# Optimization experiments

Hardware: AMD Instinct MI355X
Metric: run time of the kernel (lower is better)

The kernel has to match this reference:

```python
import jax, jax.numpy as jnp
import numpy as np
from jax import lax

B, N = 16, 4096
NPOINT, RADIUS, NSAMPLE = 1024, 0.2, 32
BN_EPS = 1e-5
MLP_DIMS = [(64, 6), (64, 64), (128, 64)]  # (C_out, C_in)


def setup_inputs() -> dict:
    key = jax.random.key(0)
    ks = jax.random.split(key, 2 + len(MLP_DIMS))
    inp = {
        "xyz": jax.random.uniform(ks[0], (B, 3, N), jnp.float32),   # unit cube
        "points": jax.random.normal(ks[1], (B, 3, N), jnp.float32),  # extra features, D=3
    }
    for i, (co, ci) in enumerate(MLP_DIMS):
        inp[f"conv_w{i}"] = jax.random.normal(ks[2 + i], (co, ci), jnp.float32) * 0.1
        inp[f"conv_b{i}"] = jnp.zeros((co,), jnp.float32)
        inp[f"bn_g{i}"] = jnp.ones((co,), jnp.float32)
        inp[f"bn_b{i}"] = jnp.zeros((co,), jnp.float32)
    return inp


def _fps(xyz, npoint):
    """Farthest point sampling. xyz: [B,N,3] -> idx [B,npoint]. Deterministic start at index 0."""
    b, n, _ = xyz.shape
    def step(carry, _):
        dist, far = carry                                  # [B,N], [B]
        c = jnp.take_along_axis(xyz, far[:, None, None], axis=1)  # [B,1,3]
        d = jnp.sum((xyz - c) ** 2, -1)                    # [B,N]
        dist = jnp.minimum(dist, d)
        return (dist, jnp.argmax(dist, -1).astype(jnp.int32)), far
    init = (jnp.full((b, n), 1e10, xyz.dtype), jnp.zeros((b,), jnp.int32))
    _, idx = lax.scan(step, init, None, length=npoint)
    return idx.T  # [B,npoint]


def _gather(pts, idx):
    """pts [B,N,C], idx [B,S,K] -> [B,S,K,C]."""
    b, s, k = idx.shape
    c = pts.shape[-1]
    flat = jnp.broadcast_to(idx.reshape(b, s * k, 1), (b, s * k, c))
    return jnp.take_along_axis(pts, flat, axis=1).reshape(b, s, k, c)


def _forward(xyz, points, params):
    xyz_t = xyz.transpose(0, 2, 1)      # [B,N,3]
    pts_t = points.transpose(0, 2, 1)   # [B,N,D]
    b, n, _ = xyz_t.shape

    fps_idx = _fps(xyz_t, NPOINT)                                       # [B,S]
    new_xyz = jnp.take_along_axis(xyz_t, fps_idx[:, :, None], axis=1)   # [B,S,3]

    # ball query: full [B,S,N] squared distances, mark out-of-ball with N, sort, take first nsample
    sqr = (jnp.sum(new_xyz ** 2, -1)[:, :, None]
           + jnp.sum(xyz_t ** 2, -1)[:, None, :]
           - 2.0 * jnp.einsum('bsc,bnc->bsn', new_xyz, xyz_t))          # [B,S,N]
    ar = jnp.arange(n, dtype=jnp.int32)
    gidx = jnp.where(sqr > RADIUS ** 2, n, ar[None, None, :])
    gidx = jnp.sort(gidx, axis=-1)[:, :, :NSAMPLE]                      # [B,S,K]
    gidx = jnp.where(gidx == n, gidx[:, :, :1], gidx)                   # pad with first neighbor

    grouped_xyz = _gather(xyz_t, gidx) - new_xyz[:, :, None, :]         # [B,S,K,3]
    grouped_pts = _gather(pts_t, gidx)                                  # [B,S,K,D]
    x = jnp.concatenate([grouped_xyz, grouped_pts], axis=-1)            # [B,S,K,6]

    for (w, bi, g, be) in params:
        x = jnp.einsum('bskc,oc->bsko', x, w) + bi                      # 1x1 conv
        m = jnp.mean(x, axis=(0, 1, 2), keepdims=True)                  # BN train-mode (biased var)
        v = jnp.var(x, axis=(0, 1, 2), keepdims=True)
        x = (x - m) * lax.rsqrt(v + BN_EPS) * g + be
        x = jax.nn.relu(x)

    new_points = jnp.max(x, axis=2)                                     # [B,S,C_last]
    return new_xyz.transpose(0, 2, 1), new_points.transpose(0, 2, 1)    # [B,3,S], [B,C,S]


def reference(xyz, points,
              conv_w0, conv_b0, bn_g0, bn_b0,
              conv_w1, conv_b1, bn_g1, bn_b1,
              conv_w2, conv_b2, bn_g2, bn_b2):
    params = [(conv_w0, conv_b0, bn_g0, bn_b0),
              (conv_w1, conv_b1, bn_g1, bn_b1),
              (conv_w2, conv_b2, bn_g2, bn_b2)]
    return _forward(xyz, points, params)
```

## Files before the change

kernel.cpp:

```cpp
#include <hip/hip_runtime.h>
#include <stdint.h>

#define NB 16
#define NN 4096
#define NS 1024
#define NK 32
#define INV_CNT (1.0f/524288.0f)
#define BN_EPS_ 1e-5f

__device__ __forceinline__ float frn_mul(float a,float b){ return __fmul_rn(a,b); }
__device__ __forceinline__ float frn_add(float a,float b){ return __fadd_rn(a,b); }
__device__ __forceinline__ float frn_sub(float a,float b){ return __fsub_rn(a,b); }

__device__ __forceinline__ unsigned long long ullmax_(unsigned long long a, unsigned long long b){ return a>b?a:b; }

typedef float v2f __attribute__((ext_vector_type(2)));

template<int CTRL>
__device__ __forceinline__ unsigned long long dpp_max_u64(unsigned long long v){
  int lo = __builtin_amdgcn_update_dpp((int)(unsigned)v, (int)(unsigned)v, CTRL, 0xf, 0xf, false);
  int hi = __builtin_amdgcn_update_dpp((int)(unsigned)(v>>32), (int)(unsigned)(v>>32), CTRL, 0xf, 0xf, false);
  unsigned long long o = (((unsigned long long)(unsigned)hi)<<32) | (unsigned long long)(unsigned)lo;
  return (o>v)?o:v;
}

__global__ __launch_bounds__(256) void k_fps(const float* __restrict__ xyz,
                                             int* __restrict__ fpsIdx,
                                             float* __restrict__ norms,
                                             float* __restrict__ outNewXyz){
  const int b = blockIdx.x;
  const float* bxp = xyz + (size_t)b*3*NN;
  const int t = threadIdx.x, lane = t&63, wv = t>>6;
  __shared__ __align__(16) float4 sxyz[NN];
  __shared__ __align__(32) unsigned long long red[2][4];
  v2f px2[8], py2[8], pz2[8], dd2[8];
  #pragma unroll
  for(int j=0;j<8;j++){
    #pragma unroll
    for(int k=0;k<2;k++){
      int n = t + (2*j+k)*256;
      float x=bxp[n], y=bxp[NN+n], z=bxp[2*NN+n];
      if(k==0){ px2[j].x=x; py2[j].x=y; pz2[j].x=z; }
      else    { px2[j].y=x; py2[j].y=y; pz2[j].y=z; }
      float nr = frn_add(frn_add(frn_mul(x,x),frn_mul(y,y)),frn_mul(z,z));
      norms[(size_t)b*NN+n]=nr;
      sxyz[n] = make_float4(x,y,z,0.f);
    }
    dd2[j].x=1e10f; dd2[j].y=1e10f;
  }
  const int rnb = NN-1-t;
  __syncthreads();
  int cur = 0;
  for(int it=0; it<NS; ++it){
    float4 c = sxyz[cur];
    if (t==0){
      fpsIdx[b*NS+it]=cur;
      outNewXyz[(size_t)b*3*NS + it]        = c.x;
      outNewXyz[(size_t)b*3*NS + NS + it]   = c.y;
      outNewXyz[(size_t)b*3*NS + 2*NS + it] = c.z;
    }
    float bestv = -1.0f; int bestr = 0;
    {
      #pragma clang fp contract(off)
      v2f cx2; cx2.x=c.x; cx2.y=c.x;
      v2f cy2; cy2.x=c.y; cy2.y=c.y;
      v2f cz2; cz2.x=c.z; cz2.y=c.z;
      #pragma unroll
      for(int j=0;j<8;j++){
        v2f dx = px2[j] - cx2;
        v2f dy = py2[j] - cy2;
        v2f dz = pz2[j] - cz2;
        v2f d  = ((dx*dx) + (dy*dy)) + (dz*dz);
        float nd0 = fminf(dd2[j].x, d.x);
        dd2[j].x = nd0;
        bool g0 = nd0 > bestv;
        bestv = g0?nd0:bestv; bestr = g0?(rnb-((2*j)<<8)):bestr;
        float nd1 = fminf(dd2[j].y, d.y);
        dd2[j].y = nd1;
        bool g1 = nd1 > bestv;
        bestv = g1?nd1:bestv; bestr = g1?(rnb-((2*j+1)<<8)):bestr;
      }
    }
    unsigned long long best = (((unsigned long long)__float_as_uint(bestv))<<32)
                            | (unsigned long long)(unsigned)bestr;
    best = dpp_max_u64<0x111>(best);
    best = dpp_max_u64<0x112>(best);
    best = dpp_max_u64<0x114>(best);
    best = dpp_max_u64<0x118>(best);
    best = dpp_max_u64<0x142>(best);
    best = dpp_max_u64<0x143>(best);
    if (lane==63) red[it&1][wv]=best;
    __syncthreads();
    unsigned long long v = ullmax_(ullmax_(red[it&1][0], red[it&1][1]),
                                   ullmax_(red[it&1][2], red[it&1][3]));
    cur = NN-1-(int)(unsigned)(v & 0xffffffffull);
    cur = __builtin_amdgcn_readfirstlane(cur);
  }
}

__global__ __launch_bounds__(256) void k_group(const float* __restrict__ xyz,
                                               const float* __restrict__ pts,
                                               const float* __restrict__ norms,
                                               const int* __restrict__ fpsIdx,
                                               float* __restrict__ grouped){
  const int t=threadIdx.x, lane=t&63, wv=t>>6;
  const int g = blockIdx.x*4 + wv;
  const int b = g>>10, s = g&1023;
  const float* bx = xyz + (size_t)b*3*NN;
  const float* bp = pts + (size_t)b*3*NN;
  int ci = __builtin_amdgcn_readfirstlane(fpsIdx[b*NS+s]);
  float cx=bx[ci], cy=bx[NN+ci], cz=bx[2*NN+ci];
  float cn2 = norms[(size_t)b*NN+ci];
  __shared__ __align__(16) float stage[4][NK][8];
  int cnt=0;
  for(int ch=0; ch<NN/64; ++ch){
    if (cnt>=NK) break;
    int n = ch*64 + lane;
    float x=bx[n], y=bx[NN+n], z=bx[2*NN+n];
    float pn2 = norms[(size_t)b*NN+n];
    float dot = frn_add(frn_add(frn_mul(cx,x),frn_mul(cy,y)),frn_mul(cz,z));
    float sqr = frn_sub(frn_add(cn2,pn2), frn_mul(2.0f,dot));
    bool ok = !(sqr > 0.04f);
    unsigned long long m = __ballot(ok);
    int pos = cnt + __popcll(m & ((1ull<<lane)-1ull));
    if (ok && pos<NK){
      float q0=bp[n], q1=bp[NN+n], q2=bp[2*NN+n];
      float* r = &stage[wv][pos][0];
      r[0]=frn_sub(x,cx); r[1]=frn_sub(y,cy); r[2]=frn_sub(z,cz);
      r[3]=q0; r[4]=q1; r[5]=q2; r[6]=0.f; r[7]=0.f;
    }
    cnt += __popcll(m);
  }
  __syncthreads();
  int c2 = cnt<NK?cnt:NK;
  if (lane>=c2 && lane<NK){
    #pragma unroll
    for(int j=0;j<8;j++) stage[wv][lane][j]=stage[wv][0][j];
  }
  __syncthreads();
  float4* dst = (float4*)(grouped + (size_t)g*NK*8);
  dst[lane] = ((const float4*)&stage[wv][0][0])[lane];
}

__device__ __forceinline__ void fma8(float* av, float4 lo, float4 hi, float w){
  av[0]=fmaf(lo.x,w,av[0]); av[1]=fmaf(lo.y,w,av[1]);
  av[2]=fmaf(lo.z,w,av[2]); av[3]=fmaf(lo.w,w,av[3]);
  av[4]=fmaf(hi.x,w,av[4]); av[5]=fmaf(hi.y,w,av[5]);
  av[6]=fmaf(hi.z,w,av[6]); av[7]=fmaf(hi.w,w,av[7]);
}

__global__ __launch_bounds__(256) void k_mlp1(const float* __restrict__ grouped,
    const float* __restrict__ w1c, const float* __restrict__ b1c,
    float* __restrict__ stats){
  const int t=threadIdx.x, lane=t&63, wv=t>>6;
  __shared__ float sAcc[128];
  __shared__ __align__(16) float h0L[4][8][12];
  for(int i=t;i<128;i+=256) sAcc[i]=0.f;
  float w1r[6];
  #pragma unroll
  for(int c=0;c<6;c++) w1r[c]=w1c[lane*6+c];
  float bias1=b1c[lane];
  __syncthreads();
  float sum0=0.f, sq0=0.f;
  const int rowBase = blockIdx.x*256 + wv*64;
  float* h0 = &h0L[wv][0][0];
  for(int bt=0; bt<8; ++bt){
    const int rb = rowBase + bt*8;
    h0[(lane&7)*12 + (lane>>3)] = grouped[(size_t)rb*8 + lane];
    __builtin_amdgcn_wave_barrier();
    float a1[8];
    #pragma unroll
    for(int r=0;r<8;r++) a1[r]=bias1;
    #pragma unroll
    for(int c=0;c<6;c++){
      float4 lo = *(const float4*)&h0[c*12+0];
      float4 hi = *(const float4*)&h0[c*12+4];
      fma8(a1, lo, hi, w1r[c]);
    }
    #pragma unroll
    for(int r=0;r<8;r++){ sum0+=a1[r]; sq0=fmaf(a1[r],a1[r],sq0); }
    __builtin_amdgcn_wave_barrier();
  }
  atomicAdd(&sAcc[lane], sum0); atomicAdd(&sAcc[64+lane], sq0);
  __syncthreads();
  for(int i=t;i<128;i+=256) atomicAdd(&stats[i], sAcc[i]);
}

__global__ __launch_bounds__(256) void k_mlp2(const float* __restrict__ grouped,
    const float* __restrict__ w1c,const float* __restrict__ b1c,
    const float* __restrict__ w2c,const float* __restrict__ b2c,
    const float* __restrict__ g1,const float* __restrict__ bb1,
    float* __restrict__ stats){
  const int t=threadIdx.x, lane=t&63, wv=t>>6;
  const int h=lane>>5, li=lane&31, c0=li, c1=li+32, r8=h*8;
  __shared__ float sAcc[128];
  __shared__ __align__(16) float h0L[4][8][20];
  __shared__ __align__(16) float h1L[4][64][20];
  __shared__ __align__(8)  float2 ws2[64][32];
  for(int i=t;i<128;i+=256) sAcc[i]=0.f;
  for(int i=t;i<2048;i+=256){
    int c=i>>5, l2=i&31;
    ws2[c][l2] = make_float2(w2c[l2*64+c], w2c[(l2+32)*64+c]);
  }

  float w1r0[6], w1r1[6];
  #pragma unroll
  for(int c=0;c<6;c++){ w1r0[c]=w1c[c0*6+c]; w1r1[c]=w1c[c1*6+c]; }
  float bias1a=b1c[c0], bias1b=b1c[c1];
  float mmA = stats[c0]*INV_CNT;
  float vvA = stats[64+c0]*INV_CNT - mmA*mmA;
  float A1a = g1[c0]*rsqrtf(vvA+BN_EPS_);
  float B1a = bb1[c0]-mmA*A1a;
  float mmB = stats[c1]*INV_CNT;
  float vvB = stats[64+c1]*INV_CNT - mmB*mmB;
  float A1b = g1[c1]*rsqrtf(vvB+BN_EPS_);
  float B1b = bb1[c1]-mmB*A1b;
  float bias2a=b2c[c0], bias2b=b2c[c1];
  __syncthreads();

  float sumA=0.f,sqA=0.f,sumB=0.f,sqB=0.f;
  const int rowBase = blockIdx.x*256 + wv*64;
  float* h0 = &h0L[wv][0][0];
  float* h1 = &h1L[wv][0][0];

  for(int bt=0; bt<4; ++bt){
    const int rb = rowBase + bt*16;
    h0[(lane&7)*20 + (lane>>3)]     = grouped[(size_t)rb*8 + lane];
    h0[(lane&7)*20 + 8 + (lane>>3)] = grouped[(size_t)(rb+8)*8 + lane];
    __builtin_amdgcn_wave_barrier();
    float a1A[8], a1B[8];
    #pragma unroll
    for(int r=0;r<8;r++){ a1A[r]=bias1a; a1B[r]=bias1b; }
    #pragma unroll
    for(int c=0;c<6;c++){
      float4 lo = *(const float4*)&h0[c*20+r8];
      float4 hi = *(const float4*)&h0[c*20+r8+4];
      fma8(a1A, lo, hi, w1r0[c]);
      fma8(a1B, lo, hi, w1r1[c]);
    }
    #pragma unroll
    for(int r=0;r<8;r++){
      a1A[r]=fmaxf(fmaf(a1A[r],A1a,B1a),0.f);
      a1B[r]=fmaxf(fmaf(a1B[r],A1b,B1b),0.f);
    }
    *(float4*)&h1[c0*20+r8]   = make_float4(a1A[0],a1A[1],a1A[2],a1A[3]);
    *(float4*)&h1[c0*20+r8+4] = make_float4(a1A[4],a1A[5],a1A[6],a1A[7]);
    *(float4*)&h1[c1*20+r8]   = make_float4(a1B[0],a1B[1],a1B[2],a1B[3]);
    *(float4*)&h1[c1*20+r8+4] = make_float4(a1B[4],a1B[5],a1B[6],a1B[7]);
    __builtin_amdgcn_wave_barrier();
    float a2A[8], a2B[8];
    #pragma unroll
    for(int r=0;r<8;r++){ a2A[r]=bias2a; a2B[r]=bias2b; }
    #pragma unroll
    for(int c=0;c<64;c++){
      float4 lo = *(const float4*)&h1[c*20+r8];
      float4 hi = *(const float4*)&h1[c*20+r8+4];
      float2 w = ws2[c][li];
      fma8(a2A, lo, hi, w.x);
      fma8(a2B, lo, hi, w.y);
    }
    #pragma unroll
    for(int r=0;r<8;r++){
      sumA+=a2A[r]; sqA=fmaf(a2A[r],a2A[r],sqA);
      sumB+=a2B[r]; sqB=fmaf(a2B[r],a2B[r],sqB);
    }
    __builtin_amdgcn_wave_barrier();
  }
  atomicAdd(&sAcc[c0], sumA); atomicAdd(&sAcc[64+c0], sqA);
  atomicAdd(&sAcc[c1], sumB); atomicAdd(&sAcc[64+c1], sqB);
  __syncthreads();
  for(int i=t;i<128;i+=256) atomicAdd(&stats[128+i], sAcc[i]);
}

__global__ __launch_bounds__(256) void k_mlp3(const float* __restrict__ grouped,
    const float* __restrict__ w1c,const float* __restrict__ b1c,
    const float* __restrict__ w2c,const float* __restrict__ b2c,
    const float* __restrict__ w3c,const float* __restrict__ b3c,
    const float* __restrict__ g1,const float* __restrict__ bb1,
    const float* __restrict__ g2,const float* __restrict__ bb2,
    const float* __restrict__ g3,
    float* __restrict__ stats,
    float* __restrict__ pre3){
  const int t=threadIdx.x, lane=t&63, wv=t>>6;
  const int h=lane>>5, li=lane&31, c0=li, c1=li+32, r8=h*8;
  __shared__ float sAcc[256];
  __shared__ __align__(16) float h0L[4][8][20];
  __shared__ __align__(16) float h1L[4][64][20];
  __shared__ __align__(16) float h2L[4][64][20];
  __shared__ __align__(8)  float2 ws2[64][32];
  for(int i=t;i<256;i+=256) sAcc[i]=0.f;
  for(int i=t;i<2048;i+=256){
    int c=i>>5, l2=i&31;
    ws2[c][l2] = make_float2(w2c[l2*64+c], w2c[(l2+32)*64+c]);
  }

  float w1r0[6], w1r1[6];
  #pragma unroll
  for(int c=0;c<6;c++){ w1r0[c]=w1c[c0*6+c]; w1r1[c]=w1c[c1*6+c]; }
  float bias1a=b1c[c0], bias1b=b1c[c1];
  float mm, vv;
  mm = stats[c0]*INV_CNT;  vv = stats[64+c0]*INV_CNT - mm*mm;
  float A1a = g1[c0]*rsqrtf(vv+BN_EPS_); float B1a = bb1[c0]-mm*A1a;
  mm = stats[c1]*INV_CNT;  vv = stats[64+c1]*INV_CNT - mm*mm;
  float A1b = g1[c1]*rsqrtf(vv+BN_EPS_); float B1b = bb1[c1]-mm*A1b;
  float bias2a=b2c[c0], bias2b=b2c[c1];
  mm = stats[128+c0]*INV_CNT; vv = stats[192+c0]*INV_CNT - mm*mm;
  float A2a = g2[c0]*rsqrtf(vv+BN_EPS_); float B2a = bb2[c0]-mm*A2a;
  mm = stats[128+c1]*INV_CNT; vv = stats[192+c1]*INV_CNT - mm*mm;
  float A2b = g2[c1]*rsqrtf(vv+BN_EPS_); float B2b = bb2[c1]-mm*A2b;
  float w3a[64], w3b[64];
  #pragma unroll
  for(int c=0;c<64;c++){ w3a[c]=w3c[lane*64+c]; w3b[c]=w3c[(lane+64)*64+c]; }
  float bias3a=b3c[lane], bias3b=b3c[lane+64];
  bool mxa=(g3[lane]>=0.f), mxb=(g3[lane+64]>=0.f);
  __syncthreads();

  float sum0=0.f,sq0=0.f,sum1=0.f,sq1=0.f;
  float e0 = mxa? -__builtin_inff(): __builtin_inff();
  float e1 = mxb? -__builtin_inff(): __builtin_inff();
  const int rowBase = blockIdx.x*256 + wv*64;
  float* h0 = &h0L[wv][0][0];
  float* h1 = &h1L[wv][0][0];
  float* h2 = &h2L[wv][0][0];

  for(int bt=0; bt<4; ++bt){
    const int rb = rowBase + bt*16;
    h0[(lane&7)*20 + (lane>>3)]     = grouped[(size_t)rb*8 + lane];
    h0[(lane&7)*20 + 8 + (lane>>3)] = grouped[(size_t)(rb+8)*8 + lane];
    __builtin_amdgcn_wave_barrier();
    float a1A[8], a1B[8];
    #pragma unroll
    for(int r=0;r<8;r++){ a1A[r]=bias1a; a1B[r]=bias1b; }
    #pragma unroll
    for(int c=0;c<6;c++){
      float4 lo = *(const float4*)&h0[c*20+r8];
      float4 hi = *(const float4*)&h0[c*20+r8+4];
      fma8(a1A, lo, hi, w1r0[c]);
      fma8(a1B, lo, hi, w1r1[c]);
    }
    #pragma unroll
    for(int r=0;r<8;r++){
      a1A[r]=fmaxf(fmaf(a1A[r],A1a,B1a),0.f);
      a1B[r]=fmaxf(fmaf(a1B[r],A1b,B1b),0.f);
    }
    *(float4*)&h1[c0*20+r8]   = make_float4(a1A[0],a1A[1],a1A[2],a1A[3]);
    *(float4*)&h1[c0*20+r8+4] = make_float4(a1A[4],a1A[5],a1A[6],a1A[7]);
    *(float4*)&h1[c1*20+r8]   = make_float4(a1B[0],a1B[1],a1B[2],a1B[3]);
    *(float4*)&h1[c1*20+r8+4] = make_float4(a1B[4],a1B[5],a1B[6],a1B[7]);
    __builtin_amdgcn_wave_barrier();
    float a2A[8], a2B[8];
    #pragma unroll
    for(int r=0;r<8;r++){ a2A[r]=bias2a; a2B[r]=bias2b; }
    #pragma unroll
    for(int c=0;c<64;c++){
      float4 lo = *(const float4*)&h1[c*20+r8];
      float4 hi = *(const float4*)&h1[c*20+r8+4];
      float2 w = ws2[c][li];
      fma8(a2A, lo, hi, w.x);
      fma8(a2B, lo, hi, w.y);
    }
    #pragma unroll
    for(int r=0;r<8;r++){
      a2A[r]=fmaxf(fmaf(a2A[r],A2a,B2a),0.f);
      a2B[r]=fmaxf(fmaf(a2B[r],A2b,B2b),0.f);
    }
    *(float4*)&h2[c0*20+r8]   = make_float4(a2A[0],a2A[1],a2A[2],a2A[3]);
    *(float4*)&h2[c0*20+r8+4] = make_float4(a2A[4],a2A[5],a2A[6],a2A[7]);
    *(float4*)&h2[c1*20+r8]   = make_float4(a2B[0],a2B[1],a2B[2],a2B[3]);
    *(float4*)&h2[c1*20+r8+4] = make_float4(a2B[4],a2B[5],a2B[6],a2B[7]);
    __builtin_amdgcn_wave_barrier();
    #pragma unroll
    for(int s=0;s<2;s++){
      float a3a[8], a3b[8];
      #pragma unroll
      for(int r=0;r<8;r++){ a3a[r]=bias3a; a3b[r]=bias3b; }
      #pragma unroll
      for(int c=0;c<64;c++){
        float4 lo = *(const float4*)&h2[c*20+s*8];
        float4 hi = *(const float4*)&h2[c*20+s*8+4];
        fma8(a3a, lo, hi, w3a[c]);
        fma8(a3b, lo, hi, w3b[c]);
      }
      #pragma unroll
      for(int r=0;r<8;r++){
        float va=a3a[r]; sum0+=va; sq0=fmaf(va,va,sq0);
        e0 = mxa? fmaxf(e0,va): fminf(e0,va);
        float vb=a3b[r]; sum1+=vb; sq1=fmaf(vb,vb,sq1);
        e1 = mxb? fmaxf(e1,vb): fminf(e1,vb);
      }
    }
    if (bt&1){
      int gg = (rowBase>>5) + (bt>>1);
      pre3[(size_t)gg*128 + lane]      = e0;
      pre3[(size_t)gg*128 + 64 + lane] = e1;
      e0 = mxa? -__builtin_inff(): __builtin_inff();
      e1 = mxb? -__builtin_inff(): __builtin_inff();
    }
    __builtin_amdgcn_wave_barrier();
  }
  atomicAdd(&sAcc[lane],      sum0);
  atomicAdd(&sAcc[64+lane],   sum1);
  atomicAdd(&sAcc[128+lane],  sq0);
  atomicAdd(&sAcc[192+lane],  sq1);
  __syncthreads();
  for(int i=t;i<128;i+=256) atomicAdd(&stats[256+i], sAcc[i]);
  for(int i=t;i<128;i+=256) atomicAdd(&stats[384+i], sAcc[128+i]);
}

__global__ __launch_bounds__(256) void k_final(const float* __restrict__ pre3,
                                               const float* __restrict__ stats,
                                               const float* __restrict__ g3,
                                               const float* __restrict__ bb3,
                                               float* __restrict__ outNP){
  __shared__ float A3[128], B3[128];
  __shared__ float til[128][65];
  const int t=threadIdx.x;
  if (t<128){
    float mm = stats[256+t]*INV_CNT;
    float vv = stats[384+t]*INV_CNT - mm*mm;
    float aa = g3[t]*rsqrtf(vv+BN_EPS_);
    A3[t]=aa; B3[t]=bb3[t]-mm*aa;
  }
  const int b = blockIdx.x>>4, s0=(blockIdx.x&15)*64;
  #pragma unroll
  for(int i=0;i<32;i++){
    int lin=i*256+t; int sl=lin>>7, o=lin&127;
    til[o][sl]=pre3[((size_t)b*NS + s0 + sl)*128 + o];
  }
  __syncthreads();
  #pragma unroll
  for(int i=0;i<32;i++){
    int lin=i*256+t; int o=lin>>6, sl=lin&63;
    outNP[(size_t)b*128*NS + (size_t)o*NS + s0 + sl] =
        fmaxf(fmaf(til[o][sl],A3[o],B3[o]),0.f);
  }
}

extern "C" void kernel_launch(void* const* d_in, const int* in_sizes, int n_in,
                              void* d_out, int out_size, void* d_ws, size_t ws_size,
                              hipStream_t stream){
  const float* xyz=(const float*)d_in[0];
  const float* pts=(const float*)d_in[1];
  const float* w1 =(const float*)d_in[2];
  const float* b1 =(const float*)d_in[3];
  const float* g1 =(const float*)d_in[4];
  const float* bb1=(const float*)d_in[5];
  const float* w2 =(const float*)d_in[6];
  const float* b2 =(const float*)d_in[7];
  const float* g2 =(const float*)d_in[8];
  const float* bb2=(const float*)d_in[9];
  const float* w3 =(const float*)d_in[10];
  const float* b3 =(const float*)d_in[11];
  const float* g3 =(const float*)d_in[12];
  const float* bb3=(const float*)d_in[13];
  float* out=(float*)d_out;
  float* outNewXyz=out;
  float* outNP=out + (size_t)NB*3*NS;

  char* ws=(char*)d_ws;
  float* stats  =(float*)ws;
  int*   fpsIdx =(int*)  (ws + 4096);
  float* norms  =(float*)(ws + 4096 + 65536);
  float* grouped=(float*)(ws + 4096 + 65536 + 262144);
  float* pre3   =(float*)(ws + 4096 + 65536 + 262144 + 16777216);

  (void)hipMemsetAsync(stats, 0, 512*sizeof(float), stream);
  k_fps  <<<dim3(NB),       dim3(256),  0, stream>>>(xyz, fpsIdx, norms, outNewXyz);
  k_group<<<dim3(NB*NS/4),  dim3(256),  0, stream>>>(xyz, pts, norms, fpsIdx, grouped);
  k_mlp1 <<<dim3(2048), dim3(256), 0, stream>>>(grouped, w1,b1, stats);
  k_mlp2 <<<dim3(2048), dim3(256), 0, stream>>>(grouped, w1,b1,w2,b2, g1,bb1, stats);
  k_mlp3 <<<dim3(2048), dim3(256), 0, stream>>>(grouped, w1,b1,w2,b2,w3,b3, g1,bb1,g2,bb2,g3, stats, pre3);
  k_final<<<dim3(256),  dim3(256), 0, stream>>>(pre3, stats, g3, bb3, outNP);
}
```

Baseline: 1.122 ms.

## Fuse layer-1 BN statistics into grouping kernel and tree-reduce FPS argmax

Drops the separate k_mlp1 kernel and computes the first conv layer's per-channel sum and sum-of-squares inside k_group, reading straight from the shared staging buffer. This saves one launch and a full re-read of the grouped buffer. Separately, the FPS per-thread argmax now packs distance and index into 64-bit keys and reduces them with a tree of max operations instead of a serial compare-select chain, which shortens the dependency chain in the serial FPS loop at the cost of more registers. The grouping kernel now does a 32-row dot loop per lane plus shared and global atomics per block, so its register use and per-block work go up.

```diff
diff --git a/kernel.cpp b/kernel.cpp
--- a/kernel.cpp
+++ b/kernel.cpp
@@ -49,6 +49,9 @@
     dd2[j].x=1e10f; dd2[j].y=1e10f;
   }
   const int rnb = NN-1-t;
+  unsigned lo16[16];
+  #pragma unroll
+  for(int i=0;i<16;i++) lo16[i] = (unsigned)(rnb - (i<<8));
   __syncthreads();
   int cur = 0;
   for(int it=0; it<NS; ++it){
@@ -59,7 +62,7 @@
       outNewXyz[(size_t)b*3*NS + NS + it]   = c.y;
       outNewXyz[(size_t)b*3*NS + 2*NS + it] = c.z;
     }
-    float bestv = -1.0f; int bestr = 0;
+    unsigned long long key[16];
     {
       #pragma clang fp contract(off)
       v2f cx2; cx2.x=c.x; cx2.y=c.x;
@@ -73,16 +76,20 @@
         v2f d  = ((dx*dx) + (dy*dy)) + (dz*dz);
         float nd0 = fminf(dd2[j].x, d.x);
         dd2[j].x = nd0;
-        bool g0 = nd0 > bestv;
-        bestv = g0?nd0:bestv; bestr = g0?(rnb-((2*j)<<8)):bestr;
+        key[2*j]   = (((unsigned long long)__float_as_uint(nd0))<<32)
+                   | (unsigned long long)lo16[2*j];
         float nd1 = fminf(dd2[j].y, d.y);
         dd2[j].y = nd1;
-        bool g1 = nd1 > bestv;
-        bestv = g1?nd1:bestv; bestr = g1?(rnb-((2*j+1)<<8)):bestr;
+        key[2*j+1] = (((unsigned long long)__float_as_uint(nd1))<<32)
+                   | (unsigned long long)lo16[2*j+1];
       }
     }
-    unsigned long long best = (((unsigned long long)__float_as_uint(bestv))<<32)
-                            | (unsigned long long)(unsigned)bestr;
+    #pragma unroll
+    for(int s=8;s>=1;s>>=1){
+      #pragma unroll
+      for(int i2=0;i2<s;i2++) key[i2]=ullmax_(key[i2],key[i2+s]);
+    }
+    unsigned long long best = key[0];
     best = dpp_max_u64<0x111>(best);
     best = dpp_max_u64<0x112>(best);
     best = dpp_max_u64<0x114>(best);
@@ -102,7 +109,10 @@
                                                const float* __restrict__ pts,
                                                const float* __restrict__ norms,
                                                const int* __restrict__ fpsIdx,
-                                               float* __restrict__ grouped){
+                                               const float* __restrict__ w1c,
+                                               const float* __restrict__ b1c,
+                                               float* __restrict__ grouped,
+                                               float* __restrict__ stats){
   const int t=threadIdx.x, lane=t&63, wv=t>>6;
   const int g = blockIdx.x*4 + wv;
   const int b = g>>10, s = g&1023;
@@ -112,6 +122,12 @@
   float cx=bx[ci], cy=bx[NN+ci], cz=bx[2*NN+ci];
   float cn2 = norms[(size_t)b*NN+ci];
   __shared__ __align__(16) float stage[4][NK][8];
+  __shared__ float sAcc[128];
+  for(int i=t;i<128;i+=256) sAcc[i]=0.f;
+  float w1r[6];
+  #pragma unroll
+  for(int c=0;c<6;c++) w1r[c]=w1c[lane*6+c];
+  float bias1=b1c[lane];
   int cnt=0;
   for(int ch=0; ch<NN/64; ++ch){
     if (cnt>=NK) break;
@@ -140,6 +156,23 @@
   __syncthreads();
   float4* dst = (float4*)(grouped + (size_t)g*NK*8);
   dst[lane] = ((const float4*)&stage[wv][0][0])[lane];
+  float sum0=0.f, sq0=0.f;
+  #pragma unroll
+  for(int r=0;r<NK;r++){
+    float4 lo4 = *(const float4*)&stage[wv][r][0];
+    float4 hi4 = *(const float4*)&stage[wv][r][4];
+    float a = bias1;
+    a = fmaf(lo4.x, w1r[0], a);
+    a = fmaf(lo4.y, w1r[1], a);
+    a = fmaf(lo4.z, w1r[2], a);
+    a = fmaf(lo4.w, w1r[3], a);
+    a = fmaf(hi4.x, w1r[4], a);
+    a = fmaf(hi4.y, w1r[5], a);
+    sum0 += a; sq0 = fmaf(a,a,sq0);
+  }
+  atomicAdd(&sAcc[lane], sum0); atomicAdd(&sAcc[64+lane], sq0);
+  __syncthreads();
+  for(int i=t;i<128;i+=256) atomicAdd(&stats[i], sAcc[i]);
 }
 
 __device__ __forceinline__ void fma8(float* av, float4 lo, float4 hi, float w){
@@ -147,43 +180,6 @@
   av[2]=fmaf(lo.z,w,av[2]); av[3]=fmaf(lo.w,w,av[3]);
   av[4]=fmaf(hi.x,w,av[4]); av[5]=fmaf(hi.y,w,av[5]);
   av[6]=fmaf(hi.z,w,av[6]); av[7]=fmaf(hi.w,w,av[7]);
-}
-
-__global__ __launch_bounds__(256) void k_mlp1(const float* __restrict__ grouped,
-    const float* __restrict__ w1c, const float* __restrict__ b1c,
-    float* __restrict__ stats){
-  const int t=threadIdx.x, lane=t&63, wv=t>>6;
-  __shared__ float sAcc[128];
-  __shared__ __align__(16) float h0L[4][8][12];
-  for(int i=t;i<128;i+=256) sAcc[i]=0.f;
-  float w1r[6];
-  #pragma unroll
-  for(int c=0;c<6;c++) w1r[c]=w1c[lane*6+c];
-  float bias1=b1c[lane];
-  __syncthreads();
-  float sum0=0.f, sq0=0.f;
-  const int rowBase = blockIdx.x*256 + wv*64;
-  float* h0 = &h0L[wv][0][0];
-  for(int bt=0; bt<8; ++bt){
-    const int rb = rowBase + bt*8;
-    h0[(lane&7)*12 + (lane>>3)] = grouped[(size_t)rb*8 + lane];
-    __builtin_amdgcn_wave_barrier();
-    float a1[8];
-    #pragma unroll
-    for(int r=0;r<8;r++) a1[r]=bias1;
-    #pragma unroll
-    for(int c=0;c<6;c++){
-      float4 lo = *(const float4*)&h0[c*12+0];
-      float4 hi = *(const float4*)&h0[c*12+4];
-      fma8(a1, lo, hi, w1r[c]);
-    }
-    #pragma unroll
-    for(int r=0;r<8;r++){ sum0+=a1[r]; sq0=fmaf(a1[r],a1[r],sq0); }
-    __builtin_amdgcn_wave_barrier();
-  }
-  atomicAdd(&sAcc[lane], sum0); atomicAdd(&sAcc[64+lane], sq0);
-  __syncthreads();
-  for(int i=t;i<128;i+=256) atomicAdd(&stats[i], sAcc[i]);
 }
 
 __global__ __launch_bounds__(256) void k_mlp2(const float* __restrict__ grouped,
@@ -466,8 +462,7 @@
 
   (void)hipMemsetAsync(stats, 0, 512*sizeof(float), stream);
   k_fps  <<<dim3(NB),       dim3(256),  0, stream>>>(xyz, fpsIdx, norms, outNewXyz);
-  k_group<<<dim3(NB*NS/4),  dim3(256),  0, stream>>>(xyz, pts, norms, fpsIdx, grouped);
-  k_mlp1 <<<dim3(2048), dim3(256), 0, stream>>>(grouped, w1,b1, stats);
+  k_group<<<dim3(NB*NS/4),  dim3(256),  0, stream>>>(xyz, pts, norms, fpsIdx, w1, b1, grouped, stats);
   k_mlp2 <<<dim3(2048), dim3(256), 0, stream>>>(grouped, w1,b1,w2,b2, g1,bb1, stats);
   k_mlp3 <<<dim3(2048), dim3(256), 0, stream>>>(grouped, w1,b1,w2,b2,w3,b3, g1,bb1,g2,bb2,g3, stats, pre3);
   k_final<<<dim3(256),  dim3(256), 0, stream>>>(pre3, stats, g3, bb3, outNP);
```

After: 1.158 ms. 3.3% more time.

## Materialize layer-2 pre-activations and split final MLP into a lighter kernel

Applied to the files above, without the earlier changes.

k_mlp2 can now write its raw layer-2 outputs (524288 rows x 64 channels) to a workspace buffer. A new k_mlp3b reads that buffer, applies BN2 and ReLU, and runs only layer 3, instead of recomputing layers 1 and 2 from the grouped input. This trades recomputation for a 128 MB write plus a 128 MB read. The new path is taken only when the workspace is large enough, otherwise the old kernels run.

```diff
diff --git a/kernel.cpp b/kernel.cpp
--- a/kernel.cpp
+++ b/kernel.cpp
@@ -186,11 +186,13 @@
   for(int i=t;i<128;i+=256) atomicAdd(&stats[i], sAcc[i]);
 }
 
+template<int STORE>
 __global__ __launch_bounds__(256) void k_mlp2(const float* __restrict__ grouped,
     const float* __restrict__ w1c,const float* __restrict__ b1c,
     const float* __restrict__ w2c,const float* __restrict__ b2c,
     const float* __restrict__ g1,const float* __restrict__ bb1,
-    float* __restrict__ stats){
+    float* __restrict__ stats,
+    float* __restrict__ h2raw){
   const int t=threadIdx.x, lane=t&63, wv=t>>6;
   const int h=lane>>5, li=lane&31, c0=li, c1=li+32, r8=h*8;
   __shared__ float sAcc[128];
@@ -264,12 +266,104 @@
       sumA+=a2A[r]; sqA=fmaf(a2A[r],a2A[r],sqA);
       sumB+=a2B[r]; sqB=fmaf(a2B[r],a2B[r],sqB);
     }
+    if constexpr (STORE){
+      #pragma unroll
+      for(int r=0;r<8;r++){
+        h2raw[(size_t)(rb + r8 + r)*64 + c0] = a2A[r];
+        h2raw[(size_t)(rb + r8 + r)*64 + c1] = a2B[r];
+      }
+    }
     __builtin_amdgcn_wave_barrier();
   }
   atomicAdd(&sAcc[c0], sumA); atomicAdd(&sAcc[64+c0], sqA);
   atomicAdd(&sAcc[c1], sumB); atomicAdd(&sAcc[64+c1], sqB);
   __syncthreads();
   for(int i=t;i<128;i+=256) atomicAdd(&stats[128+i], sAcc[i]);
+}
+
+__global__ __launch_bounds__(256) void k_mlp3b(const float* __restrict__ h2raw,
+    const float* __restrict__ w3c,const float* __restrict__ b3c,
+    const float* __restrict__ g2,const float* __restrict__ bb2,
+    const float* __restrict__ g3,
+    float* __restrict__ stats,
+    float* __restrict__ pre3){
+  const int t=threadIdx.x, lane=t&63, wv=t>>6;
+  __shared__ float sAcc[256];
+  __shared__ __align__(16) float h2L[4][64][20];
+  __shared__ float A2s[64], B2s[64];
+  for(int i=t;i<256;i+=256) sAcc[i]=0.f;
+  if (t<64){
+    float mm = stats[128+t]*INV_CNT;
+    float vv = stats[192+t]*INV_CNT - mm*mm;
+    float aa = g2[t]*rsqrtf(vv+BN_EPS_);
+    A2s[t]=aa; B2s[t]=bb2[t]-mm*aa;
+  }
+  float w3a[64], w3b[64];
+  #pragma unroll
+  for(int c=0;c<64;c++){ w3a[c]=w3c[lane*64+c]; w3b[c]=w3c[(lane+64)*64+c]; }
+  float bias3a=b3c[lane], bias3b=b3c[lane+64];
+  bool mxa=(g3[lane]>=0.f), mxb=(g3[lane+64]>=0.f);
+  __syncthreads();
+  const int lr = lane>>4;
+  const int ch4 = (lane&15)*4;
+  float A2v[4], B2v[4];
+  #pragma unroll
+  for(int jj=0;jj<4;jj++){ A2v[jj]=A2s[ch4+jj]; B2v[jj]=B2s[ch4+jj]; }
+
+  float sum0=0.f,sq0=0.f,sum1=0.f,sq1=0.f;
+  float e0 = mxa? -__builtin_inff(): __builtin_inff();
+  float e1 = mxb? -__builtin_inff(): __builtin_inff();
+  const int rowBase = blockIdx.x*256 + wv*64;
+  float* h2 = &h2L[wv][0][0];
+
+  for(int bt=0; bt<4; ++bt){
+    const int rb = rowBase + bt*16;
+    #pragma unroll
+    for(int j=0;j<4;j++){
+      int rl = j*4 + lr;
+      float4 v = *(const float4*)&h2raw[(size_t)(rb+rl)*64 + ch4];
+      h2[(ch4+0)*20 + rl] = fmaxf(fmaf(v.x, A2v[0], B2v[0]), 0.f);
+      h2[(ch4+1)*20 + rl] = fmaxf(fmaf(v.y, A2v[1], B2v[1]), 0.f);
+      h2[(ch4+2)*20 + rl] = fmaxf(fmaf(v.z, A2v[2], B2v[2]), 0.f);
+      h2[(ch4+3)*20 + rl] = fmaxf(fmaf(v.w, A2v[3], B2v[3]), 0.f);
+    }
+    __builtin_amdgcn_wave_barrier();
+    #pragma unroll
+    for(int s=0;s<2;s++){
+      float a3a[8], a3b[8];
+      #pragma unroll
+      for(int r=0;r<8;r++){ a3a[r]=bias3a; a3b[r]=bias3b; }
+      #pragma unroll
+      for(int c=0;c<64;c++){
+        float4 lo = *(const float4*)&h2[c*20+s*8];
+        float4 hi = *(const float4*)&h2[c*20+s*8+4];
+        fma8(a3a, lo, hi, w3a[c]);
+        fma8(a3b, lo, hi, w3b[c]);
+      }
+      #pragma unroll
+      for(int r=0;r<8;r++){
+        float va=a3a[r]; sum0+=va; sq0=fmaf(va,va,sq0);
+        e0 = mxa? fmaxf(e0,va): fminf(e0,va);
+        float vb=a3b[r]; sum1+=vb; sq1=fmaf(vb,vb,sq1);
+        e1 = mxb? fmaxf(e1,vb): fminf(e1,vb);
+      }
+    }
+    if (bt&1){
+      int gg = (rowBase>>5) + (bt>>1);
+      pre3[(size_t)gg*128 + lane]      = e0;
+      pre3[(size_t)gg*128 + 64 + lane] = e1;
+      e0 = mxa? -__builtin_inff(): __builtin_inff();
+      e1 = mxb? -__builtin_inff(): __builtin_inff();
+    }
+    __builtin_amdgcn_wave_barrier();
+  }
+  atomicAdd(&sAcc[lane],      sum0);
+  atomicAdd(&sAcc[64+lane],   sum1);
+  atomicAdd(&sAcc[128+lane],  sq0);
+  atomicAdd(&sAcc[192+lane],  sq1);
+  __syncthreads();
+  for(int i=t;i<128;i+=256) atomicAdd(&stats[256+i], sAcc[i]);
+  for(int i=t;i<128;i+=256) atomicAdd(&stats[384+i], sAcc[128+i]);
 }
 
 __global__ __launch_bounds__(256) void k_mlp3(const float* __restrict__ grouped,
@@ -458,17 +552,25 @@
   float* outNP=out + (size_t)NB*3*NS;
 
   char* ws=(char*)d_ws;
+  const size_t BASE = 4096 + 65536 + 262144 + 16777216 + 2097152;
   float* stats  =(float*)ws;
   int*   fpsIdx =(int*)  (ws + 4096);
   float* norms  =(float*)(ws + 4096 + 65536);
   float* grouped=(float*)(ws + 4096 + 65536 + 262144);
   float* pre3   =(float*)(ws + 4096 + 65536 + 262144 + 16777216);
+  float* h2raw  =(float*)(ws + BASE);
+  const bool split = ws_size >= BASE + 134217728ull;
 
   (void)hipMemsetAsync(stats, 0, 512*sizeof(float), stream);
   k_fps  <<<dim3(NB),       dim3(256),  0, stream>>>(xyz, fpsIdx, norms, outNewXyz);
   k_group<<<dim3(NB*NS/4),  dim3(256),  0, stream>>>(xyz, pts, norms, fpsIdx, grouped);
   k_mlp1 <<<dim3(2048), dim3(256), 0, stream>>>(grouped, w1,b1, stats);
-  k_mlp2 <<<dim3(2048), dim3(256), 0, stream>>>(grouped, w1,b1,w2,b2, g1,bb1, stats);
-  k_mlp3 <<<dim3(2048), dim3(256), 0, stream>>>(grouped, w1,b1,w2,b2,w3,b3, g1,bb1,g2,bb2,g3, stats, pre3);
+  if (split){
+    k_mlp2<1><<<dim3(2048), dim3(256), 0, stream>>>(grouped, w1,b1,w2,b2, g1,bb1, stats, h2raw);
+    k_mlp3b  <<<dim3(2048), dim3(256), 0, stream>>>(h2raw, w3,b3, g2,bb2, g3, stats, pre3);
+  } else {
+    k_mlp2<0><<<dim3(2048), dim3(256), 0, stream>>>(grouped, w1,b1,w2,b2, g1,bb1, stats, h2raw);
+    k_mlp3   <<<dim3(2048), dim3(256), 0, stream>>>(grouped, w1,b1,w2,b2,w3,b3, g1,bb1,g2,bb2,g3, stats, pre3);
+  }
   k_final<<<dim3(256),  dim3(256), 0, stream>>>(pre3, stats, g3, bb3, outNP);
 }
```

Result: faster. 1.029 ms (-8.3%).
